# Performance work log

Measured on AMD Instinct MI355X. Metric: run time of the kernel, lower is better.

## Reference

```python
import jax, jax.numpy as jnp
import numpy as np
import math

N_HEADS = 16
D_HEAD = 64
D_MODEL = 1024
ROPE_THETA = 10000.0


def setup_inputs() -> dict:
    key = jax.random.key(0)
    k1, k2, k3 = jax.random.split(key, 3)
    B, T = 2, 2048
    x = jax.random.normal(k1, (B, T, D_MODEL), dtype=jnp.float32)
    # torch Linear(in, out) weight has shape (out, in); store transposed (in, out)
    # so forward is x @ w. Scale like default init to keep activations sane.
    w_qkv = jax.random.normal(k2, (D_MODEL, 3 * D_MODEL), dtype=jnp.float32) / math.sqrt(D_MODEL)
    w_o = jax.random.normal(k3, (D_MODEL, D_MODEL), dtype=jnp.float32) / math.sqrt(D_MODEL)
    return {"x": x, "w_qkv": w_qkv, "w_o": w_o}


def _build_rope(T, dtype):
    inv_freq = 1.0 / (ROPE_THETA ** (jnp.arange(0, D_HEAD, 2, dtype=jnp.float32) / D_HEAD))
    t = jnp.arange(T, dtype=jnp.float32)
    freqs = jnp.outer(t, inv_freq)            # [T, D_HEAD/2]
    emb = jnp.concatenate([freqs, freqs], -1)  # [T, D_HEAD]
    return jnp.cos(emb).astype(dtype), jnp.sin(emb).astype(dtype)


def _apply_rope(x, cos, sin):
    # x: [B, T, H, D_HEAD]; cos/sin broadcast as [1, T, 1, D_HEAD]
    x1, x2 = jnp.split(x, 2, axis=-1)
    rotated = jnp.concatenate([-x2, x1], axis=-1)
    return x * cos + rotated * sin


def reference(x, w_qkv, w_o):
    B, T, D = x.shape
    qkv = (x @ w_qkv).reshape(B, T, 3, N_HEADS, D_HEAD)
    q, k, v = qkv[:, :, 0], qkv[:, :, 1], qkv[:, :, 2]  # [B, T, H, Dh]
    cos, sin = _build_rope(T, x.dtype)
    cos = cos[None, :, None, :]
    sin = sin[None, :, None, :]
    q = _apply_rope(q, cos, sin)
    k = _apply_rope(k, cos, sin)
    scale = 1.0 / math.sqrt(D_HEAD)
    # full [B, H, T, T] scores (faithful to the manual matmul-softmax-matmul)
    attn = jnp.einsum("bthd,bshd->bhts", q, k) * scale
    attn = jax.nn.softmax(attn, axis=-1)
    out = jnp.einsum("bhts,bshd->bthd", attn, v).reshape(B, T, D)
    return out @ w_o
```

## Files before the change

### kernel.cpp

```cpp
#include <hip/hip_runtime.h>
#include <cstdint>

typedef unsigned short ushort_t;
typedef __attribute__((ext_vector_type(8))) short v8s;
typedef __attribute__((ext_vector_type(4))) short v4s;
typedef __attribute__((ext_vector_type(2))) unsigned v2u;
typedef __attribute__((ext_vector_type(4))) float v4f;

#define MFMA(a, b, c) __builtin_amdgcn_mfma_f32_16x16x32_bf16(a, b, c, 0, 0, 0)
#define QSCALE 0.18033688011112042f

#define GLL(gp, lp) __builtin_amdgcn_global_load_lds(                        \
    (const __attribute__((address_space(1))) void*)(gp),                     \
    (__attribute__((address_space(3))) void*)(lp), 16, 0, 0)

__device__ __forceinline__ float bf2f(ushort_t u) {
    union { unsigned u; float f; } x; x.u = ((unsigned)u) << 16; return x.f;
}
__device__ __forceinline__ short f2bf(float f) {
    union { float f; unsigned u; } x; x.f = f;
    unsigned r = x.u + 0x7fffu + ((x.u >> 16) & 1u);
    return (short)(r >> 16);
}

__global__ void detect_rope(const unsigned* __restrict__ x, int* __restrict__ flag,
                            float* __restrict__ tab) {
    if (blockIdx.x == 0) {
        __shared__ int cnt;
        if (threadIdx.x == 0) cnt = 0;
        __syncthreads();
        unsigned w = x[threadIdx.x];
        int e = (w >> 7) & 0xFF;
        int hit = ((e >= 96 && e <= 135) || (w & 0xFFFFu) == 0) ? 1 : 0;
        atomicAdd(&cnt, hit);
        __syncthreads();
        if (threadIdx.x == 0) *flag = (cnt >= 160) ? 1 : 0;
    } else {
        int idx = (blockIdx.x - 1) * 256 + threadIdx.x;
        int t = idx >> 5, d = idx & 31;
        float inv_freq = __expf(-(float)d * 0.28782313662425575f);
        float ang = (float)t * inv_freq;
        float sn, cs;
        sincosf(ang, &sn, &cs);
        tab[t * 64 + d]      = bf2f((ushort_t)f2bf(cs));
        tab[t * 64 + 32 + d] = bf2f((ushort_t)f2bf(sn));
    }
}

__global__ __launch_bounds__(256) void cvt_x(const void* __restrict__ xin,
                                             ushort_t* __restrict__ xb,
                                             const int* __restrict__ flagp, int n8) {
    int i = blockIdx.x * 256 + threadIdx.x;
    if (i >= n8) return;
    if (*flagp) {
        ((v8s*)xb)[i] = ((const v8s*)xin)[i];
    } else {
        const float* xf = (const float*)xin + (size_t)i * 8;
        v8s o;
        #pragma unroll
        for (int j = 0; j < 8; ++j) o[j] = f2bf(xf[j]);
        ((v8s*)xb)[i] = o;
    }
}

__global__ __launch_bounds__(256) void cvt_transpose2(const void* __restrict__ in1,
                                                      const void* __restrict__ in2,
                                                      ushort_t* __restrict__ out1,
                                                      ushort_t* __restrict__ out2,
                                                      const int* __restrict__ flagp) {
    __shared__ ushort_t tile[32][33];
    const void* in; ushort_t* out; int C, bx;
    if (blockIdx.x < 96) { in = in1; out = out1; C = 3072; bx = blockIdx.x * 32; }
    else                 { in = in2; out = out2; C = 1024; bx = (blockIdx.x - 96) * 32; }
    const int R = 1024;
    int by = blockIdx.y * 32;
    int tx = threadIdx.x, ty = threadIdx.y;
    int isbf = *flagp;
    for (int i = ty; i < 32; i += 8) {
        size_t idx = (size_t)(by + i) * C + bx + tx;
        tile[i][tx] = isbf ? ((const ushort_t*)in)[idx]
                           : (ushort_t)f2bf(((const float*)in)[idx]);
    }
    __syncthreads();
    for (int i = ty; i < 32; i += 8) out[(size_t)(bx + i) * R + by + tx] = tile[tx][i];
}

template <int MODE, int BN>
__global__ __launch_bounds__(256) void gemm_bt(const ushort_t* __restrict__ A,
                                               const ushort_t* __restrict__ BT,
                                               void* __restrict__ C,
                                               const int* __restrict__ flagp,
                                               int M, int N, int K,
                                               ushort_t* __restrict__ Qp,
                                               ushort_t* __restrict__ Kp,
                                               ushort_t* __restrict__ Vp,
                                               const float* __restrict__ tab) {
    constexpr int NJ = BN / 32;
    __shared__ __align__(16) ushort_t As[2][128 * 32];
    __shared__ __align__(16) ushort_t Bs[2][BN * 32];
    int tid = threadIdx.x;
    int lane = tid & 63;
    int lr = lane & 15, lc = lane >> 4;
    int w = tid >> 6;
    int wr = (w >> 1) * 64, wc = (w & 1) * (BN / 2);

    int nx = gridDim.x;
    int orig = blockIdx.y * nx + blockIdx.x;
    int cpx = (nx * gridDim.y) >> 3;
    int swz = (orig & 7) * cpx + (orig >> 3);
    int m0 = (swz / nx) * 128, n0 = (swz % nx) * BN;

    int c0 = tid, c1 = tid + 256;
    int r0 = c0 >> 2, s0 = c0 & 3;
    int r1 = c1 >> 2, s1 = c1 & 3;

    const ushort_t* Ag0 = A + (size_t)(m0 + r0) * K + s0 * 8;
    const ushort_t* Ag1 = A + (size_t)(m0 + r1) * K + s1 * 8;
    const ushort_t* Bg0 = BT + (size_t)(n0 + r0) * K + s0 * 8;
    const ushort_t* Bg1 = BT + (size_t)(n0 + r1) * K + s1 * 8;
    const int aoff0 = w * 512;
    const int aoff1 = 2048 + w * 512;
    const int boff0 = w * 512;
    const int boff1 = 2048 + w * 512;

    v4f acc[4][NJ] = {};

    GLL(Ag0, &As[0][aoff0]);
    GLL(Ag1, &As[0][aoff1]);
    GLL(Bg0, &Bs[0][boff0]);
    if constexpr (BN == 128) GLL(Bg1, &Bs[0][boff1]);
    __syncthreads();

    int buf = 0;
    for (int kt = 0; kt < K; kt += 32) {
        if (kt + 32 < K) {
            int nb = buf ^ 1;
            GLL(Ag0 + kt + 32, &As[nb][aoff0]);
            GLL(Ag1 + kt + 32, &As[nb][aoff1]);
            GLL(Bg0 + kt + 32, &Bs[nb][boff0]);
            if constexpr (BN == 128) GLL(Bg1 + kt + 32, &Bs[nb][boff1]);
        }

        v8s af[4], bfr[NJ];
        #pragma unroll
        for (int i = 0; i < 4; ++i)
            af[i] = *(const v8s*)(&As[buf][0] + (wr + i * 16 + lr) * 32 + lc * 8);
        #pragma unroll
        for (int j = 0; j < NJ; ++j)
            bfr[j] = *(const v8s*)(&Bs[buf][0] + (wc + j * 16 + lr) * 32 + lc * 8);
        #pragma unroll
        for (int i = 0; i < 4; ++i)
            #pragma unroll
            for (int j = 0; j < NJ; ++j)
                acc[i][j] = MFMA(af[i], bfr[j], acc[i][j]);

        __syncthreads();
        buf ^= 1;
    }

    if (MODE == 1) {
        int store_f32 = (*flagp == 0);
        #pragma unroll
        for (int i = 0; i < 4; ++i)
            #pragma unroll
            for (int j = 0; j < NJ; ++j)
                #pragma unroll
                for (int r = 0; r < 4; ++r) {
                    int row = m0 + wr + i * 16 + lc * 4 + r;
                    int col = n0 + wc + j * 16 + lr;
                    if (store_f32)
                        ((float*)C)[(size_t)row * N + col] = acc[i][j][r];
                    else
                        ((ushort_t*)C)[(size_t)row * N + col] = (ushort_t)f2bf(acc[i][j][r]);
                }
    } else {
        int region = n0 >> 10;
        int h = ((n0 & 1023) + wc) >> 6;
        if (region < 2) {
            const float sc = (region == 0) ? QSCALE : 1.0f;
            ushort_t* dst = (region == 0) ? Qp : Kp;
            #pragma unroll
            for (int i = 0; i < 4; ++i)
                #pragma unroll
                for (int j = 0; j < 2; ++j) {
                    int d = j * 16 + lr;
                    #pragma unroll
                    for (int r = 0; r < 4; ++r) {
                        int tg = m0 + wr + i * 16 + lc * 4 + r;
                        int b = tg >> 11, tt = tg & 2047;
                        float cs = tab[tt * 64 + d], sn = tab[tt * 64 + 32 + d];
                        float x1 = acc[i][j][r], x2 = acc[i][(j + 2) % NJ][r];
                        size_t base = ((size_t)(b * 16 + h) * 2048 + tt) * 64 + d;
                        dst[base]      = (ushort_t)f2bf((x1 * cs - x2 * sn) * sc);
                        dst[base + 32] = (ushort_t)f2bf((x2 * cs + x1 * sn) * sc);
                    }
                }
        } else {
            #pragma unroll
            for (int i = 0; i < 4; ++i)
                #pragma unroll
                for (int j = 0; j < NJ; ++j) {
                    int d = j * 16 + lr;
                    int tg0 = m0 + wr + i * 16 + lc * 4;
                    int b = tg0 >> 11, tt = tg0 & 2047;
                    v4s pk;
                    #pragma unroll
                    for (int r = 0; r < 4; ++r) pk[r] = f2bf(acc[i][j][r]);
                    size_t base = (size_t)(b * 16 + h) * 131072 + (size_t)(tt >> 5) * 2048
                                + (size_t)d * 32 + (tt & 31);
                    *(v4s*)(Vp + base) = pk;
                }
        }
    }
}

__global__ __launch_bounds__(256) void attn(const ushort_t* __restrict__ Qr,
                                            const ushort_t* __restrict__ Kr,
                                            const ushort_t* __restrict__ Vt,
                                            ushort_t* __restrict__ AO) {
    __shared__ __align__(16) char lds[53248];
    int tid = threadIdx.x, lane = tid & 63, W = tid >> 6;
    int lr = lane & 15, lc = lane >> 4;
    int qsub = W & 1, sh = W >> 1;
    int L = blockIdx.x;
    int bh = (L & 7) * 4 + ((L >> 3) & 3);
    int qt = L >> 5;
    int q0 = qt * 128 + qsub * 64;
    int b = bh >> 4, h = bh & 15;
    const ushort_t* Qb = Qr + ((size_t)bh * 2048 + q0) * 64;
    const ushort_t* Kb = Kr + (size_t)bh * 131072 + (size_t)sh * 65536;
    const ushort_t* Vb = Vt + (size_t)bh * 131072 + (size_t)sh * 65536;
    ushort_t* Pw  = (ushort_t*)(lds + 32768 + W * 5120);
    ushort_t* KsG = (ushort_t*)(lds + sh * 16384);
    ushort_t* VsG = (ushort_t*)(lds + sh * 16384 + 8192);

    int gt = tid & 127;
    int c0 = gt, c1 = gt + 128;
    int kr0 = c0 >> 3, kc0 = c0 & 7, kr1 = c1 >> 3, kc1 = c1 & 7;
    const ushort_t* Kg0 = Kb + (size_t)kr0 * 64 + kc0 * 8;
    const ushort_t* Kg1 = Kb + (size_t)kr1 * 64 + kc1 * 8;
    int kl0 = kr0 * 64 + (kc0 ^ (kr0 & 7)) * 8;
    int kl1 = kr1 * 64 + (kc1 ^ (kr1 & 7)) * 8;
    const ushort_t* Vg0 = Vb + (size_t)c0 * 8;
    const ushort_t* Vg1 = Vb + (size_t)c1 * 8;
    int vl0 = c0 * 8, vl1 = c1 * 8;

    v8s qf[4][2];
    #pragma unroll
    for (int jq = 0; jq < 4; ++jq)
        #pragma unroll
        for (int kk = 0; kk < 2; ++kk)
            qf[jq][kk] = *(const v8s*)(Qb + (size_t)(jq * 16 + lr) * 64 + kk * 32 + lc * 8);

    v4f o[4][4] = {};
    float li[4] = {0.f, 0.f, 0.f, 0.f};

    v8s ka = *(const v8s*)(Kg0), kb2 = *(const v8s*)(Kg1);
    v8s va = *(const v8s*)(Vg0), vb2 = *(const v8s*)(Vg1);
    *(v8s*)(KsG + kl0) = ka;
    *(v8s*)(KsG + kl1) = kb2;
    *(v8s*)(VsG + vl0) = va;
    *(v8s*)(VsG + vl1) = vb2;
    ka  = *(const v8s*)(Kg0 + 2048);
    kb2 = *(const v8s*)(Kg1 + 2048);
    va  = *(const v8s*)(Vg0 + 2048);
    vb2 = *(const v8s*)(Vg1 + 2048);
    __syncthreads();

    #pragma unroll 1
    for (int t = 0; t < 32; ++t) {
        int p = t & 1;
        const ushort_t* Kl = KsG + p * 2048;
        const ushort_t* Vl = VsG + p * 2048;

        v8s kf[2][2], vf[4];
        #pragma unroll
        for (int hh = 0; hh < 2; ++hh)
            #pragma unroll
            for (int kk = 0; kk < 2; ++kk)
                kf[hh][kk] = *(const v8s*)(Kl + (hh * 16 + lr) * 64 + (((kk * 4 + lc) ^ (lr & 7)) * 8));
        #pragma unroll
        for (int i = 0; i < 4; ++i)
            vf[i] = *(const v8s*)(Vl + (i * 16 + lr) * 32 + lc * 8);

        v4f St[2][4] = {};
        __builtin_amdgcn_s_setprio(1);
        #pragma unroll
        for (int hh = 0; hh < 2; ++hh)
            #pragma unroll
            for (int jq = 0; jq < 4; ++jq) {
                St[hh][jq] = MFMA(kf[hh][0], qf[jq][0], St[hh][jq]);
                St[hh][jq] = MFMA(kf[hh][1], qf[jq][1], St[hh][jq]);
            }
        __builtin_amdgcn_s_setprio(0);

        if (t + 1 < 32) {
            ushort_t* Kn = KsG + (p ^ 1) * 2048;
            ushort_t* Vn = VsG + (p ^ 1) * 2048;
            *(v8s*)(Kn + kl0) = ka;
            *(v8s*)(Kn + kl1) = kb2;
            *(v8s*)(Vn + vl0) = va;
            *(v8s*)(Vn + vl1) = vb2;
        }
        if (t + 2 < 32) {
            ka  = *(const v8s*)(Kg0 + (size_t)(t + 2) * 2048);
            kb2 = *(const v8s*)(Kg1 + (size_t)(t + 2) * 2048);
            va  = *(const v8s*)(Vg0 + (size_t)(t + 2) * 2048);
            vb2 = *(const v8s*)(Vg1 + (size_t)(t + 2) * 2048);
        }

        #pragma unroll
        for (int jq = 0; jq < 4; ++jq)
            #pragma unroll
            for (int hh = 0; hh < 2; ++hh) {
                #pragma unroll
                for (int r = 0; r < 4; ++r) {
                    float ev = __builtin_amdgcn_exp2f(St[hh][jq][r]);
                    St[hh][jq][r] = ev;
                    li[jq] += ev;
                }
                unsigned d0 = __builtin_amdgcn_perm(__float_as_uint(St[hh][jq][1]),
                                                    __float_as_uint(St[hh][jq][0]), 0x07060302u);
                unsigned d1 = __builtin_amdgcn_perm(__float_as_uint(St[hh][jq][3]),
                                                    __float_as_uint(St[hh][jq][2]), 0x07060302u);
                v2u pk = {d0, d1};
                *(v2u*)(Pw + (jq * 16 + lr) * 40 + hh * 16 + lc * 4) = pk;
            }
        __builtin_amdgcn_s_waitcnt(0xc07f);
        __builtin_amdgcn_s_setprio(1);
        #pragma unroll
        for (int jq = 0; jq < 4; ++jq) {
            v8s pf = *(const v8s*)(Pw + (jq * 16 + lr) * 40 + lc * 8);
            #pragma unroll
            for (int i = 0; i < 4; ++i)
                o[i][jq] = MFMA(vf[i], pf, o[i][jq]);
        }
        __builtin_amdgcn_s_setprio(0);
        __syncthreads();
    }

    #pragma unroll
    for (int jq = 0; jq < 4; ++jq) {
        li[jq] += __shfl_xor(li[jq], 16);
        li[jq] += __shfl_xor(li[jq], 32);
    }
    float* MO = (float*)(lds + qsub * 17408);
    float* Ml = (float*)(lds + 34816 + qsub * 256);
    __syncthreads();
    if (sh == 1) {
        #pragma unroll
        for (int jq = 0; jq < 4; ++jq) {
            #pragma unroll
            for (int i = 0; i < 4; ++i)
                *(v4f*)(MO + (jq * 16 + lr) * 68 + i * 16 + lc * 4) = o[i][jq];
            if (lc == 0) Ml[jq * 16 + lr] = li[jq];
        }
    }
    __syncthreads();
    if (sh == 0) {
        #pragma unroll
        for (int jq = 0; jq < 4; ++jq) {
            float inv = 1.0f / (li[jq] + Ml[jq * 16 + lr]);
            int t = q0 + jq * 16 + lr;
            #pragma unroll
            for (int i = 0; i < 4; ++i) {
                v4f m = *(const v4f*)(MO + (jq * 16 + lr) * 68 + i * 16 + lc * 4);
                v4s pk;
                #pragma unroll
                for (int r = 0; r < 4; ++r) pk[r] = f2bf((o[i][jq][r] + m[r]) * inv);
                *(v4s*)(AO + (size_t)(b * 2048 + t) * 1024 + h * 64 + i * 16 + lc * 4) = pk;
            }
        }
    }
}

extern "C" void kernel_launch(void* const* d_in, const int* in_sizes, int n_in,
                              void* d_out, int out_size, void* d_ws, size_t ws_size,
                              hipStream_t stream) {
    char* ws = (char*)d_ws;
    int*      flag  = (int*)ws;
    ushort_t* wqkvT = (ushort_t*)(ws + 256);
    ushort_t* woT   = (ushort_t*)(ws + 6291712);
    ushort_t* xb    = (ushort_t*)(ws + 8388864);
    ushort_t* Qr    = (ushort_t*)(ws + 16777472);
    ushort_t* Kr    = (ushort_t*)(ws + 25166080);
    ushort_t* Vt    = (ushort_t*)(ws + 33554688);
    ushort_t* AO    = (ushort_t*)(ws + 41943296);
    float*    tab   = (float*)(ws + 50331904);

    detect_rope<<<257, 256, 0, stream>>>((const unsigned*)d_in[0], flag, tab);
    cvt_x<<<2048, 256, 0, stream>>>(d_in[0], xb, flag, 524288);
    dim3 tb(32, 8);
    cvt_transpose2<<<dim3(128, 32), tb, 0, stream>>>(d_in[1], d_in[2], wqkvT, woT, flag);
    gemm_bt<2, 128><<<dim3(24, 32), 256, 0, stream>>>(xb, wqkvT, nullptr, flag, 4096, 3072, 1024,
                                                      Qr, Kr, Vt, tab);
    attn<<<512, 256, 0, stream>>>(Qr, Kr, Vt, AO);
    gemm_bt<1, 64><<<dim3(16, 32), 256, 0, stream>>>(AO, woT, d_out, flag, 4096, 1024, 1024,
                                                     nullptr, nullptr, nullptr, nullptr);
}
```

Baseline: 191.6 us.

## Split attention keys four ways per block, load K/V directly from global

The attention kernel now gives each of the four waves in a block the same 64 queries and a quarter of the key range. Each wave reads its K/V fragments straight from global memory with register prefetch, which removes the shared-memory staging and the per-iteration block barrier. The grid doubles to 1024 blocks and a three-way LDS reduction merges the partial outputs and row sums. The weight transpose kernel also moves to 64x64 tiles with 64x4 threads. This trades LDS reuse of K/V across waves for more global/L2 traffic and a larger final reduction.

```diff
diff --git a/kernel.cpp b/kernel.cpp
--- a/kernel.cpp
+++ b/kernel.cpp
@@ -68,21 +68,21 @@
                                                       ushort_t* __restrict__ out1,
                                                       ushort_t* __restrict__ out2,
                                                       const int* __restrict__ flagp) {
-    __shared__ ushort_t tile[32][33];
+    __shared__ ushort_t tile[64][65];
     const void* in; ushort_t* out; int C, bx;
-    if (blockIdx.x < 96) { in = in1; out = out1; C = 3072; bx = blockIdx.x * 32; }
-    else                 { in = in2; out = out2; C = 1024; bx = (blockIdx.x - 96) * 32; }
+    if (blockIdx.x < 48) { in = in1; out = out1; C = 3072; bx = blockIdx.x * 64; }
+    else                 { in = in2; out = out2; C = 1024; bx = (blockIdx.x - 48) * 64; }
     const int R = 1024;
-    int by = blockIdx.y * 32;
+    int by = blockIdx.y * 64;
     int tx = threadIdx.x, ty = threadIdx.y;
     int isbf = *flagp;
-    for (int i = ty; i < 32; i += 8) {
+    for (int i = ty; i < 64; i += 4) {
         size_t idx = (size_t)(by + i) * C + bx + tx;
         tile[i][tx] = isbf ? ((const ushort_t*)in)[idx]
                            : (ushort_t)f2bf(((const float*)in)[idx]);
     }
     __syncthreads();
-    for (int i = ty; i < 32; i += 8) out[(size_t)(bx + i) * R + by + tx] = tile[tx][i];
+    for (int i = ty; i < 64; i += 4) out[(size_t)(bx + i) * R + by + tx] = tile[tx][i];
 }
 
 template <int MODE, int BN>
@@ -221,29 +221,26 @@
     __shared__ __align__(16) char lds[53248];
     int tid = threadIdx.x, lane = tid & 63, W = tid >> 6;
     int lr = lane & 15, lc = lane >> 4;
-    int qsub = W & 1, sh = W >> 1;
+    int sh = W;
     int L = blockIdx.x;
     int bh = (L & 7) * 4 + ((L >> 3) & 3);
     int qt = L >> 5;
-    int q0 = qt * 128 + qsub * 64;
+    int q0 = qt * 64;
     int b = bh >> 4, h = bh & 15;
     const ushort_t* Qb = Qr + ((size_t)bh * 2048 + q0) * 64;
-    const ushort_t* Kb = Kr + (size_t)bh * 131072 + (size_t)sh * 65536;
-    const ushort_t* Vb = Vt + (size_t)bh * 131072 + (size_t)sh * 65536;
-    ushort_t* Pw  = (ushort_t*)(lds + 32768 + W * 5120);
-    ushort_t* KsG = (ushort_t*)(lds + sh * 16384);
-    ushort_t* VsG = (ushort_t*)(lds + sh * 16384 + 8192);
-
-    int gt = tid & 127;
-    int c0 = gt, c1 = gt + 128;
-    int kr0 = c0 >> 3, kc0 = c0 & 7, kr1 = c1 >> 3, kc1 = c1 & 7;
-    const ushort_t* Kg0 = Kb + (size_t)kr0 * 64 + kc0 * 8;
-    const ushort_t* Kg1 = Kb + (size_t)kr1 * 64 + kc1 * 8;
-    int kl0 = kr0 * 64 + (kc0 ^ (kr0 & 7)) * 8;
-    int kl1 = kr1 * 64 + (kc1 ^ (kr1 & 7)) * 8;
-    const ushort_t* Vg0 = Vb + (size_t)c0 * 8;
-    const ushort_t* Vg1 = Vb + (size_t)c1 * 8;
-    int vl0 = c0 * 8, vl1 = c1 * 8;
+    const ushort_t* Kp = Kr + (size_t)bh * 131072 + (size_t)sh * 32768;
+    const ushort_t* Vp = Vt + (size_t)bh * 131072 + (size_t)sh * 32768;
+    ushort_t* Pw = (ushort_t*)(lds + W * 5120);
+
+    int kO[2][2], vO[4];
+    #pragma unroll
+    for (int hh = 0; hh < 2; ++hh)
+        #pragma unroll
+        for (int kk = 0; kk < 2; ++kk)
+            kO[hh][kk] = (hh * 16 + lr) * 64 + (kk * 4 + lc) * 8;
+    #pragma unroll
+    for (int i = 0; i < 4; ++i)
+        vO[i] = (i * 16 + lr) * 32 + lc * 8;
 
     v8s qf[4][2];
     #pragma unroll
@@ -255,34 +252,18 @@
     v4f o[4][4] = {};
     float li[4] = {0.f, 0.f, 0.f, 0.f};
 
-    v8s ka = *(const v8s*)(Kg0), kb2 = *(const v8s*)(Kg1);
-    v8s va = *(const v8s*)(Vg0), vb2 = *(const v8s*)(Vg1);
-    *(v8s*)(KsG + kl0) = ka;
-    *(v8s*)(KsG + kl1) = kb2;
-    *(v8s*)(VsG + vl0) = va;
-    *(v8s*)(VsG + vl1) = vb2;
-    ka  = *(const v8s*)(Kg0 + 2048);
-    kb2 = *(const v8s*)(Kg1 + 2048);
-    va  = *(const v8s*)(Vg0 + 2048);
-    vb2 = *(const v8s*)(Vg1 + 2048);
-    __syncthreads();
+    v8s kf[2][2], vf[4];
+    #pragma unroll
+    for (int hh = 0; hh < 2; ++hh)
+        #pragma unroll
+        for (int kk = 0; kk < 2; ++kk)
+            kf[hh][kk] = *(const v8s*)(Kp + kO[hh][kk]);
+    #pragma unroll
+    for (int i = 0; i < 4; ++i)
+        vf[i] = *(const v8s*)(Vp + vO[i]);
 
     #pragma unroll 1
-    for (int t = 0; t < 32; ++t) {
-        int p = t & 1;
-        const ushort_t* Kl = KsG + p * 2048;
-        const ushort_t* Vl = VsG + p * 2048;
-
-        v8s kf[2][2], vf[4];
-        #pragma unroll
-        for (int hh = 0; hh < 2; ++hh)
-            #pragma unroll
-            for (int kk = 0; kk < 2; ++kk)
-                kf[hh][kk] = *(const v8s*)(Kl + (hh * 16 + lr) * 64 + (((kk * 4 + lc) ^ (lr & 7)) * 8));
-        #pragma unroll
-        for (int i = 0; i < 4; ++i)
-            vf[i] = *(const v8s*)(Vl + (i * 16 + lr) * 32 + lc * 8);
-
+    for (int t = 0; t < 16; ++t) {
         v4f St[2][4] = {};
         __builtin_amdgcn_s_setprio(1);
         #pragma unroll
@@ -294,19 +275,12 @@
             }
         __builtin_amdgcn_s_setprio(0);
 
-        if (t + 1 < 32) {
-            ushort_t* Kn = KsG + (p ^ 1) * 2048;
-            ushort_t* Vn = VsG + (p ^ 1) * 2048;
-            *(v8s*)(Kn + kl0) = ka;
-            *(v8s*)(Kn + kl1) = kb2;
-            *(v8s*)(Vn + vl0) = va;
-            *(v8s*)(Vn + vl1) = vb2;
-        }
-        if (t + 2 < 32) {
-            ka  = *(const v8s*)(Kg0 + (size_t)(t + 2) * 2048);
-            kb2 = *(const v8s*)(Kg1 + (size_t)(t + 2) * 2048);
-            va  = *(const v8s*)(Vg0 + (size_t)(t + 2) * 2048);
-            vb2 = *(const v8s*)(Vg1 + (size_t)(t + 2) * 2048);
+        if (t < 15) {
+            #pragma unroll
+            for (int hh = 0; hh < 2; ++hh)
+                #pragma unroll
+                for (int kk = 0; kk < 2; ++kk)
+                    kf[hh][kk] = *(const v8s*)(Kp + 2048 + kO[hh][kk]);
         }
 
         #pragma unroll
@@ -336,7 +310,13 @@
                 o[i][jq] = MFMA(vf[i], pf, o[i][jq]);
         }
         __builtin_amdgcn_s_setprio(0);
-        __syncthreads();
+
+        if (t < 15) {
+            #pragma unroll
+            for (int i = 0; i < 4; ++i)
+                vf[i] = *(const v8s*)(Vp + 2048 + vO[i]);
+        }
+        Kp += 2048; Vp += 2048;
     }
 
     #pragma unroll
@@ -344,31 +324,37 @@
         li[jq] += __shfl_xor(li[jq], 16);
         li[jq] += __shfl_xor(li[jq], 32);
     }
-    float* MO = (float*)(lds + qsub * 17408);
-    float* Ml = (float*)(lds + 34816 + qsub * 256);
+
+    float* Ml = (float*)(lds + 52224);
     __syncthreads();
-    if (sh == 1) {
+    if (W != 0) {
+        float* MO = (float*)(lds + (W - 1) * 17408);
         #pragma unroll
         for (int jq = 0; jq < 4; ++jq) {
             #pragma unroll
             for (int i = 0; i < 4; ++i)
                 *(v4f*)(MO + (jq * 16 + lr) * 68 + i * 16 + lc * 4) = o[i][jq];
-            if (lc == 0) Ml[jq * 16 + lr] = li[jq];
+            if (lc == 0) Ml[(W - 1) * 64 + jq * 16 + lr] = li[jq];
         }
     }
     __syncthreads();
-    if (sh == 0) {
+    if (W == 0) {
         #pragma unroll
         for (int jq = 0; jq < 4; ++jq) {
-            float inv = 1.0f / (li[jq] + Ml[jq * 16 + lr]);
-            int t = q0 + jq * 16 + lr;
+            int row = jq * 16 + lr;
+            float ls = li[jq] + Ml[row] + Ml[64 + row] + Ml[128 + row];
+            float inv = 1.0f / ls;
+            int tq = q0 + row;
             #pragma unroll
             for (int i = 0; i < 4; ++i) {
-                v4f m = *(const v4f*)(MO + (jq * 16 + lr) * 68 + i * 16 + lc * 4);
+                v4f m0v = *(const v4f*)((float*)(lds + 0 * 17408) + row * 68 + i * 16 + lc * 4);
+                v4f m1v = *(const v4f*)((float*)(lds + 1 * 17408) + row * 68 + i * 16 + lc * 4);
+                v4f m2v = *(const v4f*)((float*)(lds + 2 * 17408) + row * 68 + i * 16 + lc * 4);
                 v4s pk;
                 #pragma unroll
-                for (int r = 0; r < 4; ++r) pk[r] = f2bf((o[i][jq][r] + m[r]) * inv);
-                *(v4s*)(AO + (size_t)(b * 2048 + t) * 1024 + h * 64 + i * 16 + lc * 4) = pk;
+                for (int r = 0; r < 4; ++r)
+                    pk[r] = f2bf((o[i][jq][r] + m0v[r] + m1v[r] + m2v[r]) * inv);
+                *(v4s*)(AO + (size_t)(b * 2048 + tq) * 1024 + h * 64 + i * 16 + lc * 4) = pk;
             }
         }
     }
@@ -390,11 +376,10 @@
 
     detect_rope<<<257, 256, 0, stream>>>((const unsigned*)d_in[0], flag, tab);
     cvt_x<<<2048, 256, 0, stream>>>(d_in[0], xb, flag, 524288);
-    dim3 tb(32, 8);
-    cvt_transpose2<<<dim3(128, 32), tb, 0, stream>>>(d_in[1], d_in[2], wqkvT, woT, flag);
+    cvt_transpose2<<<dim3(64, 16), dim3(64, 4), 0, stream>>>(d_in[1], d_in[2], wqkvT, woT, flag);
     gemm_bt<2, 128><<<dim3(24, 32), 256, 0, stream>>>(xb, wqkvT, nullptr, flag, 4096, 3072, 1024,
                                                       Qr, Kr, Vt, tab);
-    attn<<<512, 256, 0, stream>>>(Qr, Kr, Vt, AO);
+    attn<<<1024, 256, 0, stream>>>(Qr, Kr, Vt, AO);
     gemm_bt<1, 64><<<dim3(16, 32), 256, 0, stream>>>(AO, woT, d_out, flag, 4096, 1024, 1024,
                                                      nullptr, nullptr, nullptr, nullptr);
 }
```

Result: slower. 197.0 us (+2.8%).
